# Kernel optimization log

Hardware: AMD Instinct MI355X
Metric: run time of the kernel (lower is better)

## Reference

```python
import jax, jax.numpy as jnp
import numpy as np

IN_CH, OUT_CH, K, STRIDE, PAD, NUM_POINTS = 16, 32, 3, 1, 1, 3
NUM_INPUTS = IN_CH * K * K  # 144
BATCH, H, W = 8, 32, 32


def setup_inputs() -> dict:
    key = jax.random.key(0)
    k1, k2, k3 = jax.random.split(key, 3)
    x = jax.random.normal(k1, (BATCH, IN_CH, H, W), dtype=jnp.float32)
    # sorted breakpoint positions per (input, output) pair in [-1, 1]
    base = jnp.linspace(-1.0, 1.0, NUM_POINTS, dtype=jnp.float32)
    jitter = 0.2 * (jax.random.uniform(k2, (NUM_INPUTS, OUT_CH, NUM_POINTS), dtype=jnp.float32) - 0.5) / NUM_POINTS
    positions = jnp.sort(base[None, None, :] + jitter, axis=-1)  # (I, O, P), sorted
    values = 0.1 * jax.random.normal(k3, (NUM_INPUTS, OUT_CH, NUM_POINTS), dtype=jnp.float32)
    return {"x": x, "positions": positions, "values": values}


def _gather_pt(table, idx):
    # table: (I, O, P), idx: (N, I, O) -> (N, I, O)
    return jnp.take_along_axis(table[None], idx[..., None], axis=-1)[..., 0]


def _piecewise(patches, positions, values):
    # patches: (N, I); positions/values: (I, O, P)
    P = positions.shape[-1]
    # bucket index: number of breakpoints <= x, clipped to a valid segment
    cmp = patches[:, :, None, None] >= positions[None]       # (N, I, O, P)
    idx = jnp.clip(cmp.sum(axis=-1) - 1, 0, P - 2)           # (N, I, O)
    pl = _gather_pt(positions, idx)
    pr = _gather_pt(positions, idx + 1)
    vl = _gather_pt(values, idx)
    vr = _gather_pt(values, idx + 1)
    t = (patches[:, :, None] - pl) / (pr - pl)               # (N, I, O)
    y = vl + t * (vr - vl)                                   # per-pair piecewise-linear value
    return y.sum(axis=1)                                     # (N, O): sum over input dims


def reference(x, positions, values):
    B, C, Hi, Wi = x.shape
    Ho = (Hi + 2 * PAD - K) // STRIDE + 1
    Wo = (Wi + 2 * PAD - K) // STRIDE + 1
    # im2col / unfold: (B, C*K*K, Ho, Wo) with (c, kh, kw) feature ordering like torch unfold
    patches = jax.lax.conv_general_dilated_patches(
        x, (K, K), (STRIDE, STRIDE), ((PAD, PAD), (PAD, PAD)))
    patches = patches.reshape(B, NUM_INPUTS, Ho * Wo).transpose(0, 2, 1).reshape(-1, NUM_INPUTS)
    out = _piecewise(patches, positions, values)             # (B*Ho*Wo, O)
    out = out.reshape(B, Ho * Wo, OUT_CH).transpose(0, 2, 1)
    return out.reshape(B, OUT_CH, Ho, Wo)
```

## Files before the change

### kernel.cpp

```cpp
#include <hip/hip_runtime.h>

#define IN_CH 16
#define OUT_CH 32
#define NUM_INPUTS 144
#define H_ 32
#define W_ 32
#define TILE_H 8
#define LDS_H 10
#define LDS_W 34
#define CHW (LDS_H * LDS_W)

typedef __attribute__((ext_vector_type(2))) float f32x2;

__global__ __launch_bounds__(256) void apc_fused(
        const float* __restrict__ x,
        const float* __restrict__ pos,
        const float* __restrict__ val,
        float* __restrict__ out) {
    __shared__ float lx[IN_CH * CHW];
    __shared__ float lt[2 * NUM_INPUTS * 8];

    int bx  = blockIdx.x;
    int b   = bx >> 2;
    int ho0 = (bx & 3) * TILE_H;
    int g   = blockIdx.y;
    int tid = threadIdx.x;

    for (int idx = tid; idx < IN_CH * CHW; idx += 256) {
        int c   = idx / CHW;
        int rem = idx - c * CHW;
        int r   = rem / LDS_W;
        int col = rem - r * LDS_W;
        int gr  = ho0 + r - 1;
        int gc  = col - 1;
        float v = 0.f;
        if ((unsigned)gr < (unsigned)H_ && (unsigned)gc < (unsigned)W_)
            v = x[((b * IN_CH + c) * H_ + gr) * W_ + gc];
        lx[idx] = v;
    }

    if (tid < NUM_INPUTS) {
        const float4* pp = (const float4*)(pos + tid * 96 + g * 12);
        const float4* vv = (const float4*)(val + tid * 96 + g * 12);
        float4 pA = pp[0], pB = pp[1], pC = pp[2];
        float4 vA = vv[0], vB = vv[1], vC = vv[2];
        float P[12] = {pA.x,pA.y,pA.z,pA.w, pB.x,pB.y,pB.z,pB.w, pC.x,pC.y,pC.z,pC.w};
        float V[12] = {vA.x,vA.y,vA.z,vA.w, vB.x,vB.y,vB.z,vB.w, vC.x,vC.y,vC.z,vC.w};
        float p1[4], m0[4], dm[4], b0[4];
        #pragma unroll
        for (int k = 0; k < 4; ++k) {
            float q0 = P[3*k], q1 = P[3*k+1], q2 = P[3*k+2];
            float w0 = V[3*k], w1 = V[3*k+1], w2 = V[3*k+2];
            float s0 = (w1 - w0) / (q1 - q0);
            float s1 = (w2 - w1) / (q2 - q1);
            p1[k] = q1; m0[k] = s0; dm[k] = s1 - s0; b0[k] = w0 - s0 * q0;
        }
        float4* d0 = (float4*)&lt[tid * 8];
        d0[0] = make_float4(p1[0], p1[1], m0[0], m0[1]);
        d0[1] = make_float4(dm[0], dm[1], b0[0], b0[1]);
        float4* d1 = (float4*)&lt[(NUM_INPUTS + tid) * 8];
        d1[0] = make_float4(p1[2], p1[3], m0[2], m0[3]);
        d1[1] = make_float4(dm[2], dm[3], b0[2], b0[3]);
    }
    __syncthreads();

    int col  = tid & 31;
    int trow = (tid >> 5) & 3;
    int pgrp = tid >> 7;
    int base = (2 * trow) * LDS_W + col;
    const float* tb = &lt[pgrp * NUM_INPUTS * 8];

    f32x2 aA = {0,0}, hA = {0,0};
    f32x2 aB = {0,0}, hB = {0,0};
    f32x2 bb = {0,0};
    const f32x2 zz = {0.f, 0.f};

    #pragma unroll
    for (int c = 0; c < IN_CH; ++c) {
        #pragma unroll
        for (int kw = 0; kw < 3; ++kw) {
            float p0 = lx[c * CHW + base + 0 * LDS_W + kw];
            float p1 = lx[c * CHW + base + 1 * LDS_W + kw];
            float p2 = lx[c * CHW + base + 2 * LDS_W + kw];
            float p3 = lx[c * CHW + base + 3 * LDS_W + kw];
            float pa[4] = {p0, p1, p2, p3};
            #pragma unroll
            for (int kh = 0; kh < 3; ++kh) {
                int i = (c * 3 + kh) * 3 + kw;
                float4 q0 = *(const float4*)(tb + i * 8);
                float4 q1 = *(const float4*)(tb + i * 8 + 4);
                f32x2 P = {q0.x, q0.y}, M = {q0.z, q0.w};
                f32x2 D = {q1.x, q1.y}, B = {q1.z, q1.w};
                f32x2 qA = {pa[kh],     pa[kh]};
                f32x2 qB = {pa[kh + 1], pa[kh + 1]};
                aA = __builtin_elementwise_fma(M, qA, aA);
                hA = __builtin_elementwise_fma(D, __builtin_elementwise_max(qA - P, zz), hA);
                aB = __builtin_elementwise_fma(M, qB, aB);
                hB = __builtin_elementwise_fma(D, __builtin_elementwise_max(qB - P, zz), hB);
                bb += B;
            }
        }
    }

    f32x2 rA = aA + hA + bb;
    f32x2 rB = aB + hB + bb;

    int hoA = ho0 + 2 * trow;
    int o0  = 4 * g + 2 * pgrp;
    int HW  = H_ * W_;
    int ob  = ((b * OUT_CH + o0) * H_ + hoA) * W_ + col;
    out[ob         ] = rA.x;
    out[ob +     HW] = rA.y;
    out[ob + W_            ] = rB.x;
    out[ob + W_ +       HW ] = rB.y;
}

extern "C" void kernel_launch(void* const* d_in, const int* in_sizes, int n_in,
                              void* d_out, int out_size, void* d_ws, size_t ws_size,
                              hipStream_t stream) {
    const float* x   = (const float*)d_in[0];
    const float* pos = (const float*)d_in[1];
    const float* val = (const float*)d_in[2];

    dim3 grid(32, 8);
    apc_fused<<<grid, 256, 0, stream>>>(x, pos, val, (float*)d_out);
}
```

Measured before the change: 71.77 us.

## Split input channels across thread halves, halve row tile, and reduce partials in LDS

The row tile shrinks from 8 to 4 and the grid doubles to 512 blocks. Inside each block the 16 input channels are split into two halves, handled by the two thread groups, and their partial sums are combined through shared memory before one half writes the output. The constant bias term is now precomputed once per thread with a wavefront shuffle reduction instead of being accumulated inside the inner loop, and the table is split into separate arrays so the unused bias is no longer loaded per iteration. In exchange the kernel pays for an extra barrier, an LDS reduction, and duplicated halo loads, with only half the threads doing the final store.

```diff
diff --git a/kernel.cpp b/kernel.cpp
--- a/kernel.cpp
+++ b/kernel.cpp
@@ -5,24 +5,27 @@
 #define NUM_INPUTS 144
 #define H_ 32
 #define W_ 32
-#define TILE_H 8
-#define LDS_H 10
+#define TILE_H 4
+#define LDS_H 6
 #define LDS_W 34
 #define CHW (LDS_H * LDS_W)
 
 typedef __attribute__((ext_vector_type(2))) float f32x2;
 
-__global__ __launch_bounds__(256) void apc_fused(
+__global__ __launch_bounds__(256, 2) void apc_fused(
         const float* __restrict__ x,
         const float* __restrict__ pos,
         const float* __restrict__ val,
         float* __restrict__ out) {
-    __shared__ float lx[IN_CH * CHW];
-    __shared__ float lt[2 * NUM_INPUTS * 8];
+    __shared__ float  lx[IN_CH * CHW];
+    __shared__ float4 ltPM[2 * NUM_INPUTS];
+    __shared__ f32x2  ltD [2 * NUM_INPUTS];
+    __shared__ f32x2  ltB [2 * NUM_INPUTS];
+    __shared__ float4 lred[128];
 
     int bx  = blockIdx.x;
-    int b   = bx >> 2;
-    int ho0 = (bx & 3) * TILE_H;
+    int b   = bx >> 3;
+    int ho0 = (bx & 7) * TILE_H;
     int g   = blockIdx.y;
     int tid = threadIdx.x;
 
@@ -55,28 +58,39 @@
             float s1 = (w2 - w1) / (q2 - q1);
             p1[k] = q1; m0[k] = s0; dm[k] = s1 - s0; b0[k] = w0 - s0 * q0;
         }
-        float4* d0 = (float4*)&lt[tid * 8];
-        d0[0] = make_float4(p1[0], p1[1], m0[0], m0[1]);
-        d0[1] = make_float4(dm[0], dm[1], b0[0], b0[1]);
-        float4* d1 = (float4*)&lt[(NUM_INPUTS + tid) * 8];
-        d1[0] = make_float4(p1[2], p1[3], m0[2], m0[3]);
-        d1[1] = make_float4(dm[2], dm[3], b0[2], b0[3]);
+        ltPM[tid]              = make_float4(p1[0], p1[1], m0[0], m0[1]);
+        ltD [tid]              = (f32x2){dm[0], dm[1]};
+        ltB [tid]              = (f32x2){b0[0], b0[1]};
+        ltPM[NUM_INPUTS + tid] = make_float4(p1[2], p1[3], m0[2], m0[3]);
+        ltD [NUM_INPUTS + tid] = (f32x2){dm[2], dm[3]};
+        ltB [NUM_INPUTS + tid] = (f32x2){b0[2], b0[3]};
     }
     __syncthreads();
 
     int col  = tid & 31;
-    int trow = (tid >> 5) & 3;
-    int pgrp = tid >> 7;
+    int trow = (tid >> 5) & 1;
+    int pgrp = (tid >> 6) & 1;
+    int cs   = tid >> 7;
+    int i0   = cs * 72;
+    int tb0  = pgrp * NUM_INPUTS + i0;
     int base = (2 * trow) * LDS_W + col;
-    const float* tb = &lt[pgrp * NUM_INPUTS * 8];
+    int lane = tid & 63;
+
+    f32x2 bb = ltB[tb0 + lane];
+    if (lane < 8) bb += ltB[tb0 + 64 + lane];
+    #pragma unroll
+    for (int m = 1; m < 64; m <<= 1) {
+        bb.x += __shfl_xor(bb.x, m);
+        bb.y += __shfl_xor(bb.y, m);
+    }
 
     f32x2 aA = {0,0}, hA = {0,0};
     f32x2 aB = {0,0}, hB = {0,0};
-    f32x2 bb = {0,0};
     const f32x2 zz = {0.f, 0.f};
 
     #pragma unroll
-    for (int c = 0; c < IN_CH; ++c) {
+    for (int cc = 0; cc < 8; ++cc) {
+        int c = cs * 8 + cc;
         #pragma unroll
         for (int kw = 0; kw < 3; ++kw) {
             float p0 = lx[c * CHW + base + 0 * LDS_W + kw];
@@ -86,18 +100,16 @@
             float pa[4] = {p0, p1, p2, p3};
             #pragma unroll
             for (int kh = 0; kh < 3; ++kh) {
-                int i = (c * 3 + kh) * 3 + kw;
-                float4 q0 = *(const float4*)(tb + i * 8);
-                float4 q1 = *(const float4*)(tb + i * 8 + 4);
-                f32x2 P = {q0.x, q0.y}, M = {q0.z, q0.w};
-                f32x2 D = {q1.x, q1.y}, B = {q1.z, q1.w};
+                int ti = pgrp * NUM_INPUTS + (c * 3 + kh) * 3 + kw;
+                float4 q = ltPM[ti];
+                f32x2  D = ltD[ti];
+                f32x2  P = {q.x, q.y}, M = {q.z, q.w};
                 f32x2 qA = {pa[kh],     pa[kh]};
                 f32x2 qB = {pa[kh + 1], pa[kh + 1]};
                 aA = __builtin_elementwise_fma(M, qA, aA);
                 hA = __builtin_elementwise_fma(D, __builtin_elementwise_max(qA - P, zz), hA);
                 aB = __builtin_elementwise_fma(M, qB, aB);
                 hB = __builtin_elementwise_fma(D, __builtin_elementwise_max(qB - P, zz), hB);
-                bb += B;
             }
         }
     }
@@ -105,14 +117,21 @@
     f32x2 rA = aA + hA + bb;
     f32x2 rB = aB + hB + bb;
 
-    int hoA = ho0 + 2 * trow;
-    int o0  = 4 * g + 2 * pgrp;
-    int HW  = H_ * W_;
-    int ob  = ((b * OUT_CH + o0) * H_ + hoA) * W_ + col;
-    out[ob         ] = rA.x;
-    out[ob +     HW] = rA.y;
-    out[ob + W_            ] = rB.x;
-    out[ob + W_ +       HW ] = rB.y;
+    if (cs == 1)
+        lred[tid - 128] = make_float4(rA.x, rA.y, rB.x, rB.y);
+    __syncthreads();
+    if (cs == 0) {
+        float4 q = lred[tid];
+        rA.x += q.x; rA.y += q.y; rB.x += q.z; rB.y += q.w;
+        int hoA = ho0 + 2 * trow;
+        int o0  = 4 * g + 2 * pgrp;
+        int HW  = H_ * W_;
+        int ob  = ((b * OUT_CH + o0) * H_ + hoA) * W_ + col;
+        out[ob          ] = rA.x;
+        out[ob +      HW] = rA.y;
+        out[ob + W_     ] = rB.x;
+        out[ob + W_ + HW] = rB.y;
+    }
 }
 
 extern "C" void kernel_launch(void* const* d_in, const int* in_sizes, int n_in,
@@ -122,6 +141,6 @@
     const float* pos = (const float*)d_in[1];
     const float* val = (const float*)d_in[2];
 
-    dim3 grid(32, 8);
+    dim3 grid(64, 8);
     apc_fused<<<grid, 256, 0, stream>>>(x, pos, val, (float*)d_out);
 }
```

Measured after the change: 66.87 us (median of 2 runs). 6.8% less time.
